# Kernel optimization log

Hardware: AMD Instinct MI355X
Metric: run time of the kernel (lower is better)

## Reference

```python
import jax, jax.numpy as jnp
import numpy as np

B, S, D, H, DH, SD = 4, 512, 768, 12, 64, 30
ALPHA, BETA = 1.0, 1.0


def setup_inputs() -> dict:
    root = jax.random.key(0)
    ks = jax.random.split(root, 16)
    n = lambda k, sh: jax.random.normal(k, sh, dtype=jnp.float32)
    w = lambda k, sh: 0.02 * jax.random.normal(k, sh, dtype=jnp.float32)
    return {
        "key": n(ks[0], (B, S, D)),
        "value": n(ks[1], (B, S, D)),
        "query": n(ks[2], (B, S, D)),
        "structure": n(ks[3], (B, S, S, SD)),
        "mask": jax.random.randint(ks[4], (B, S, S), 0, 2).astype(bool),
        "Wq": w(ks[5], (D, D)), "bq": jnp.zeros((D,), jnp.float32),
        "Wk": w(ks[6], (D, D)), "bk": jnp.zeros((D,), jnp.float32),
        "Wv": w(ks[7], (D, D)), "bv": jnp.zeros((D,), jnp.float32),
        "Wsk": w(ks[8], (SD, DH)), "bsk": jnp.zeros((DH,), jnp.float32),
        "Wsv": w(ks[9], (SD, DH)), "bsv": jnp.zeros((DH,), jnp.float32),
        "Wo": w(ks[10], (D, D)), "bo": jnp.zeros((D,), jnp.float32),
    }


def reference(key, value, query, structure, mask,
              Wq, bq, Wk, bk, Wv, bv, Wsk, bsk, Wsv, bsv, Wo, bo):
    # shape: [B,S,D] -> [B,H,S,DH]
    def proj(x, W, b):
        return (x @ W + b).reshape(B, -1, H, DH).transpose(0, 2, 1, 3)

    q = proj(query, Wq, bq) / np.float32(np.sqrt(DH))  # scale applied before both score terms
    k = proj(key, Wk, bk)
    v = proj(value, Wv, bv)

    sk = structure @ Wsk + bsk  # [B,Q,K,DH] relative-structure keys
    sv = structure @ Wsv + bsv  # [B,Q,K,DH] relative-structure values

    scores = jnp.einsum('bhqd,bhkd->bhqk', q, k)
    scores = scores + ALPHA * jnp.einsum('bhqd,bqkd->bhqk', q, sk)
    scores = jnp.where(mask[:, None, :, :], jnp.float32(-1e18), scores)

    attn = jax.nn.softmax(scores, axis=-1)  # dropout p=0 -> identity

    ctx = jnp.einsum('bhqk,bhkd->bhqd', attn, v)
    ctx = ctx + BETA * jnp.einsum('bhqk,bqkd->bhqd', attn, sv)
    ctx = ctx.transpose(0, 2, 1, 3).reshape(B, S, D)

    output = ctx @ Wo + bo
    top_attn = attn[:, 0]  # [B,Q,K]
    return output, top_attn
```

## Files before the change

### kernel.cpp

```cpp
#include <hip/hip_runtime.h>
#include <hip/hip_bf16.h>

typedef unsigned int uint32_ty;

typedef float  nfloat2 __attribute__((ext_vector_type(2)));
typedef float  nfloat4 __attribute__((ext_vector_type(4)));
typedef int    nint4   __attribute__((ext_vector_type(4)));
typedef short  bf16x8  __attribute__((ext_vector_type(8)));
typedef float  f32x4   __attribute__((ext_vector_type(4)));
typedef unsigned short ushort4n __attribute__((ext_vector_type(4)));

#define BB 4
#define SS 512
#define DD 768
#define HH 12
#define DHH 64
#define SDD 30

#define LP 520

__device__ __forceinline__ float bfu(unsigned short u) {
    return __uint_as_float(((uint32_ty)u) << 16);
}
__device__ __forceinline__ unsigned short tobf(float f) {
    return __bfloat16_as_ushort(__float2bfloat16(f));
}
__device__ __forceinline__ void unp8(uint4 u, float* t) {
    t[0] = __uint_as_float(u.x << 16);
    t[1] = __uint_as_float(u.x & 0xFFFF0000u);
    t[2] = __uint_as_float(u.y << 16);
    t[3] = __uint_as_float(u.y & 0xFFFF0000u);
    t[4] = __uint_as_float(u.z << 16);
    t[5] = __uint_as_float(u.z & 0xFFFF0000u);
    t[6] = __uint_as_float(u.w << 16);
    t[7] = __uint_as_float(u.w & 0xFFFF0000u);
}
__device__ __forceinline__ void unp4(uint2 u, float* t) {
    t[0] = __uint_as_float(u.x << 16);
    t[1] = __uint_as_float(u.x & 0xFFFF0000u);
    t[2] = __uint_as_float(u.y << 16);
    t[3] = __uint_as_float(u.y & 0xFFFF0000u);
}

#define MBM 64
#define MBN 64
#define MBK 64
#define LDK 72

__global__ __launch_bounds__(256) void gemm_proj3(
    const float* __restrict__ Xq, const float* __restrict__ Xk, const float* __restrict__ Xv,
    const float* __restrict__ Wq, const float* __restrict__ Wk, const float* __restrict__ Wv,
    const float* __restrict__ bq, const float* __restrict__ bk, const float* __restrict__ bv,
    float* __restrict__ oq, unsigned short* __restrict__ okT, unsigned short* __restrict__ ov)
{
    __shared__ unsigned short As[MBM][LDK];
    __shared__ unsigned short Bs[MBN][LDK];
    int z = blockIdx.z;
    const float* X = (z == 0) ? Xq : (z == 1) ? Xk : Xv;
    const float* W = (z == 0) ? Wq : (z == 1) ? Wk : Wv;
    const float* bias = (z == 0) ? bq : (z == 1) ? bk : bv;

    int tid = threadIdx.x;
    int lane = tid & 63, wave = tid >> 6;
    int m0 = blockIdx.y * MBM, n0 = blockIdx.x * MBN;
    int wm = (wave >> 1) * 32, wn = (wave & 1) * 32;
    int fr = lane & 15, fq = lane >> 4;

    f32x4 acc[2][2];
#pragma unroll
    for (int i = 0; i < 2; i++)
#pragma unroll
        for (int j = 0; j < 2; j++) acc[i][j] = (f32x4){0.f, 0.f, 0.f, 0.f};

    for (int k0 = 0; k0 < DD; k0 += MBK) {
#pragma unroll
        for (int rep = 0; rep < 4; rep++) {
            int i = tid + 256 * rep;
            int r = i >> 4, c4 = i & 15;
            float4 xv = *(const float4*)(X + (size_t)(m0 + r) * DD + k0 + 4 * c4);
            ushort4n pk = {tobf(xv.x), tobf(xv.y), tobf(xv.z), tobf(xv.w)};
            *(ushort4n*)&As[r][4 * c4] = pk;
        }
#pragma unroll
        for (int rep = 0; rep < 4; rep++) {
            int i = tid + 256 * rep;
            int r = i >> 4, c4 = i & 15;
            float4 wv = *(const float4*)(W + (size_t)(k0 + r) * DD + n0 + 4 * c4);
            Bs[4 * c4 + 0][r] = tobf(wv.x);
            Bs[4 * c4 + 1][r] = tobf(wv.y);
            Bs[4 * c4 + 2][r] = tobf(wv.z);
            Bs[4 * c4 + 3][r] = tobf(wv.w);
        }
        __syncthreads();
#pragma unroll
        for (int ks = 0; ks < 2; ks++) {
            bf16x8 a0 = *(bf16x8*)&As[wm + fr][ks * 32 + fq * 8];
            bf16x8 a1 = *(bf16x8*)&As[wm + 16 + fr][ks * 32 + fq * 8];
            bf16x8 b0 = *(bf16x8*)&Bs[wn + fr][ks * 32 + fq * 8];
            bf16x8 b1 = *(bf16x8*)&Bs[wn + 16 + fr][ks * 32 + fq * 8];
            acc[0][0] = __builtin_amdgcn_mfma_f32_16x16x32_bf16(a0, b0, acc[0][0], 0, 0, 0);
            acc[0][1] = __builtin_amdgcn_mfma_f32_16x16x32_bf16(a0, b1, acc[0][1], 0, 0, 0);
            acc[1][0] = __builtin_amdgcn_mfma_f32_16x16x32_bf16(a1, b0, acc[1][0], 0, 0, 0);
            acc[1][1] = __builtin_amdgcn_mfma_f32_16x16x32_bf16(a1, b1, acc[1][1], 0, 0, 0);
        }
        __syncthreads();
    }

#pragma unroll
    for (int i = 0; i < 2; i++) {
#pragma unroll
        for (int j = 0; j < 2; j++) {
            int n = n0 + wn + 16 * j + fr;
            int h = n >> 6, d = n & 63;
            float bn = bias[n];
            int mbase = m0 + wm + 16 * i + fq * 4;
            int b = mbase >> 9, sbase = mbase & 511;
            if (z == 1) {
                ushort4n pk;
#pragma unroll
                for (int r = 0; r < 4; r++) pk[r] = tobf(acc[i][j][r] + bn);
                *(ushort4n*)(okT + ((((size_t)b * HH + h) * DHH + d) * SS + sbase)) = pk;
            } else if (z == 0) {
#pragma unroll
                for (int r = 0; r < 4; r++)
                    oq[((((size_t)b * HH + h) * SS + sbase + r) * DHH + d)] =
                        (acc[i][j][r] + bn) * 0.125f;
            } else {
#pragma unroll
                for (int r = 0; r < 4; r++)
                    ov[((((size_t)b * HH + h) * SS + sbase + r) * DHH + d)] =
                        tobf(acc[i][j][r] + bn);
            }
        }
    }
}

__global__ __launch_bounds__(256) void gemm_out(
    const float* __restrict__ Xf, const float* __restrict__ W,
    const float* __restrict__ bias, float* __restrict__ out)
{
    __shared__ unsigned short As[MBM][LDK];
    __shared__ unsigned short Bs[MBN][LDK];
    int tid = threadIdx.x;
    int lane = tid & 63, wave = tid >> 6;
    int m0 = blockIdx.y * MBM, n0 = blockIdx.x * MBN;
    int wm = (wave >> 1) * 32, wn = (wave & 1) * 32;
    int fr = lane & 15, fq = lane >> 4;

    f32x4 acc[2][2];
#pragma unroll
    for (int i = 0; i < 2; i++)
#pragma unroll
        for (int j = 0; j < 2; j++) acc[i][j] = (f32x4){0.f, 0.f, 0.f, 0.f};

    for (int k0 = 0; k0 < DD; k0 += MBK) {
#pragma unroll
        for (int rep = 0; rep < 4; rep++) {
            int i = tid + 256 * rep;
            int r = i >> 4, c4 = i & 15;
            float4 xv = *(const float4*)(Xf + (size_t)(m0 + r) * DD + k0 + 4 * c4);
            ushort4n pk = {tobf(xv.x), tobf(xv.y), tobf(xv.z), tobf(xv.w)};
            *(ushort4n*)&As[r][4 * c4] = pk;
        }
#pragma unroll
        for (int rep = 0; rep < 4; rep++) {
            int i = tid + 256 * rep;
            int r = i >> 4, c4 = i & 15;
            float4 wv = *(const float4*)(W + (size_t)(k0 + r) * DD + n0 + 4 * c4);
            Bs[4 * c4 + 0][r] = tobf(wv.x);
            Bs[4 * c4 + 1][r] = tobf(wv.y);
            Bs[4 * c4 + 2][r] = tobf(wv.z);
            Bs[4 * c4 + 3][r] = tobf(wv.w);
        }
        __syncthreads();
#pragma unroll
        for (int ks = 0; ks < 2; ks++) {
            bf16x8 a0 = *(bf16x8*)&As[wm + fr][ks * 32 + fq * 8];
            bf16x8 a1 = *(bf16x8*)&As[wm + 16 + fr][ks * 32 + fq * 8];
            bf16x8 b0 = *(bf16x8*)&Bs[wn + fr][ks * 32 + fq * 8];
            bf16x8 b1 = *(bf16x8*)&Bs[wn + 16 + fr][ks * 32 + fq * 8];
            acc[0][0] = __builtin_amdgcn_mfma_f32_16x16x32_bf16(a0, b0, acc[0][0], 0, 0, 0);
            acc[0][1] = __builtin_amdgcn_mfma_f32_16x16x32_bf16(a0, b1, acc[0][1], 0, 0, 0);
            acc[1][0] = __builtin_amdgcn_mfma_f32_16x16x32_bf16(a1, b0, acc[1][0], 0, 0, 0);
            acc[1][1] = __builtin_amdgcn_mfma_f32_16x16x32_bf16(a1, b1, acc[1][1], 0, 0, 0);
        }
        __syncthreads();
    }

#pragma unroll
    for (int i = 0; i < 2; i++) {
#pragma unroll
        for (int j = 0; j < 2; j++) {
            int n = n0 + wn + 16 * j + fr;
            float bn = bias[n];
            int mbase = m0 + wm + 16 * i + fq * 4;
#pragma unroll
            for (int r = 0; r < 4; r++)
                out[(size_t)(mbase + r) * DD + n] = acc[i][j][r] + bn;
        }
    }
}

__global__ __launch_bounds__(256) void attn_fused(
    const float* __restrict__ q,
    const unsigned short* __restrict__ kT,
    const unsigned short* __restrict__ v,
    const float* __restrict__ structure,
    const int* __restrict__ mask,
    const float* __restrict__ Wsk,
    const float* __restrict__ bsk,
    const float* __restrict__ Wsv,
    const float* __restrict__ bsv,
    float* __restrict__ ctx,
    float* __restrict__ top_attn)
{
    __shared__ float qs[HH][DHH];
    __shared__ unsigned short stT[SDD][LP];
    __shared__ float qt_s[HH][SDD];
    __shared__ float qb_s[HH];
    __shared__ float astr_s[HH][SDD];
    __shared__ unsigned short at[HH][LP];

    int tid = threadIdx.x;
    int lane = tid & 63, wave = tid >> 6;

    int blk = blockIdx.x;
    int xcd = blk & 7;
    int b = xcd >> 1;
    int qp = ((xcd & 1) << 8) | (blk >> 3);

    for (int i = tid; i < HH * DHH; i += 256) {
        int h = i >> 6, d = i & 63;
        qs[h][d] = q[(((size_t)b * HH + h) * SS + qp) * DHH + d];
    }
    {
        const float* srow = structure + ((size_t)b * SS + qp) * (size_t)(SS * SDD);
        for (int k = tid; k < SS; k += 256) {
            const nfloat2* rp = (const nfloat2*)(srow + (size_t)k * SDD);
#pragma unroll
            for (int w = 0; w < 15; w++) {
                nfloat2 xv = __builtin_nontemporal_load(rp + w);
                stT[2 * w][k] = tobf(xv.x);
                stT[2 * w + 1][k] = tobf(xv.y);
            }
        }
    }
    __syncthreads();

    for (int i = tid; i < HH * SDD; i += 256) {
        int h = i / SDD, si = i % SDD;
        const float4* wp = (const float4*)(Wsk + si * DHH);
        const float4* qp4 = (const float4*)qs[h];
        float a = 0.f;
#pragma unroll
        for (int d4 = 0; d4 < 16; d4++) {
            float4 wv = wp[d4];
            float4 qv = qp4[d4];
            a += qv.x * wv.x + qv.y * wv.y + qv.z * wv.z + qv.w * wv.w;
        }
        qt_s[h][si] = a;
    }
    if (tid < HH) {
        const float4* bp = (const float4*)bsk;
        const float4* qp4 = (const float4*)qs[tid];
        float a = 0.f;
#pragma unroll
        for (int d4 = 0; d4 < 16; d4++) {
            float4 wv = bp[d4];
            float4 qv = qp4[d4];
            a += qv.x * wv.x + qv.y * wv.y + qv.z * wv.z + qv.w * wv.w;
        }
        qb_s[tid] = a;
    }
    __syncthreads();

    int h0 = wave * 3;
    float attnv[3][8];
#pragma unroll
    for (int h = 0; h < 3; h++)
#pragma unroll
        for (int j = 0; j < 8; j++) attnv[h][j] = 0.f;

#pragma unroll 2
    for (int si = 0; si < SDD; si++) {
        uint4 sv4 = *(const uint4*)&stT[si][8 * lane];
        float t[8];
        unp8(sv4, t);
#pragma unroll
        for (int h = 0; h < 3; h++) {
            float qt = qt_s[h0 + h][si];
#pragma unroll
            for (int j = 0; j < 8; j++) attnv[h][j] += qt * t[j];
        }
    }

    {
        const unsigned short* kbase = kT + (((size_t)b * HH + h0) * DHH) * SS + 8 * lane;
#pragma unroll
        for (int h = 0; h < 3; h++) {
            const unsigned short* kp = kbase + (size_t)h * (DHH * SS);
            float acc[8] = {0.f, 0.f, 0.f, 0.f, 0.f, 0.f, 0.f, 0.f};
#pragma unroll 8
            for (int d = 0; d < DHH; d++) {
                float qd = qs[h0 + h][d];
                uint4 kv = *(const uint4*)(kp + (size_t)d * SS);
                float t[8];
                unp8(kv, t);
#pragma unroll
                for (int j = 0; j < 8; j++) acc[j] += qd * t[j];
            }
            float qb = qb_s[h0 + h];
#pragma unroll
            for (int j = 0; j < 8; j++) attnv[h][j] += acc[j] + qb;
        }
    }

    {
        const int* mrow = mask + ((size_t)b * SS + qp) * SS + 8 * lane;
        nint4 m0v = __builtin_nontemporal_load((const nint4*)mrow);
        nint4 m1v = __builtin_nontemporal_load(((const nint4*)mrow) + 1);
        int mm[8] = {m0v.x, m0v.y, m0v.z, m0v.w, m1v.x, m1v.y, m1v.z, m1v.w};
#pragma unroll
        for (int h = 0; h < 3; h++)
#pragma unroll
            for (int j = 0; j < 8; j++)
                if (mm[j]) attnv[h][j] = -1e18f;
    }

#pragma unroll
    for (int h = 0; h < 3; h++) {
        float m = attnv[h][0];
#pragma unroll
        for (int j = 1; j < 8; j++) m = fmaxf(m, attnv[h][j]);
#pragma unroll
        for (int off = 32; off > 0; off >>= 1) m = fmaxf(m, __shfl_xor(m, off));
        float l = 0.f;
#pragma unroll
        for (int j = 0; j < 8; j++) { attnv[h][j] = __expf(attnv[h][j] - m); l += attnv[h][j]; }
#pragma unroll
        for (int off = 32; off > 0; off >>= 1) l += __shfl_xor(l, off);
        float inv = 1.f / l;
        float a[8];
#pragma unroll
        for (int j = 0; j < 8; j++) a[j] = attnv[h][j] * inv;
        uint4 pk;
        pk.x = (uint32_ty)tobf(a[0]) | ((uint32_ty)tobf(a[1]) << 16);
        pk.y = (uint32_ty)tobf(a[2]) | ((uint32_ty)tobf(a[3]) << 16);
        pk.z = (uint32_ty)tobf(a[4]) | ((uint32_ty)tobf(a[5]) << 16);
        pk.w = (uint32_ty)tobf(a[6]) | ((uint32_ty)tobf(a[7]) << 16);
        *(uint4*)&at[h0 + h][8 * lane] = pk;
        if (h0 + h == 0) {
            float* tp = top_attn + ((size_t)b * SS + qp) * SS + 8 * lane;
            nfloat4 w0 = {a[0], a[1], a[2], a[3]};
            nfloat4 w1 = {a[4], a[5], a[6], a[7]};
            __builtin_nontemporal_store(w0, (nfloat4*)tp);
            __builtin_nontemporal_store(w1, ((nfloat4*)tp) + 1);
        }
    }
    __syncthreads();

    if (tid < 180) {
        int h = tid / 15, sp = tid % 15;
        int si0 = 2 * sp, si1 = si0 + 1;
        float a0e = 0.f, a0o = 0.f, a1e = 0.f, a1o = 0.f;
#pragma unroll 2
        for (int j = 0; j < 64; j++) {
            uint4 av = *(const uint4*)&at[h][8 * j];
            uint4 s0 = *(const uint4*)&stT[si0][8 * j];
            uint4 s1 = *(const uint4*)&stT[si1][8 * j];
            float a[8], t0[8], t1[8];
            unp8(av, a); unp8(s0, t0); unp8(s1, t1);
#pragma unroll
            for (int t = 0; t < 8; t += 2) {
                a0e += a[t] * t0[t];     a0o += a[t + 1] * t0[t + 1];
                a1e += a[t] * t1[t];     a1o += a[t + 1] * t1[t + 1];
            }
        }
        astr_s[h][si0] = a0e + a0o;
        astr_s[h][si1] = a1e + a1o;
    }
    __syncthreads();

    if (tid < 192) {
        int h = tid >> 4, dq = tid & 15;
        const unsigned short* vp = v + ((size_t)b * HH + h) * (size_t)(SS * DHH) + 4 * dq;
        float4 ae; ae.x = ae.y = ae.z = ae.w = 0.f;
        float4 ao; ao.x = ao.y = ao.z = ao.w = 0.f;
#pragma unroll 2
        for (int j = 0; j < 64; j++) {
            uint4 av = *(const uint4*)&at[h][8 * j];
            float a[8];
            unp8(av, a);
            const unsigned short* vk = vp + (size_t)(8 * j) * DHH;
#pragma unroll
            for (int t = 0; t < 8; t += 2) {
                uint2 v0 = *(const uint2*)(vk + (size_t)t * DHH);
                uint2 v1 = *(const uint2*)(vk + (size_t)(t + 1) * DHH);
                float f0[4], f1[4];
                unp4(v0, f0); unp4(v1, f1);
                ae.x += a[t] * f0[0]; ae.y += a[t] * f0[1];
                ae.z += a[t] * f0[2]; ae.w += a[t] * f0[3];
                ao.x += a[t + 1] * f1[0]; ao.y += a[t + 1] * f1[1];
                ao.z += a[t + 1] * f1[2]; ao.w += a[t + 1] * f1[3];
            }
        }
        float4 sa = *(const float4*)(bsv + 4 * dq);
#pragma unroll
        for (int si = 0; si < SDD; si++) {
            float as = astr_s[h][si];
            float4 wv = *(const float4*)(Wsv + si * DHH + 4 * dq);
            sa.x += as * wv.x; sa.y += as * wv.y;
            sa.z += as * wv.z; sa.w += as * wv.w;
        }
        float4 outv;
        outv.x = ae.x + ao.x + sa.x;
        outv.y = ae.y + ao.y + sa.y;
        outv.z = ae.z + ao.z + sa.z;
        outv.w = ae.w + ao.w + sa.w;
        *(float4*)(ctx + ((size_t)b * SS + qp) * DD + h * DHH + 4 * dq) = outv;
    }
}

extern "C" void kernel_launch(void* const* d_in, const int* in_sizes, int n_in,
                              void* d_out, int out_size, void* d_ws, size_t ws_size,
                              hipStream_t stream)
{
    const float* key       = (const float*)d_in[0];
    const float* value     = (const float*)d_in[1];
    const float* query     = (const float*)d_in[2];
    const float* structure = (const float*)d_in[3];
    const int*   mask      = (const int*)d_in[4];
    const float* Wq  = (const float*)d_in[5];
    const float* bq  = (const float*)d_in[6];
    const float* Wk  = (const float*)d_in[7];
    const float* bk  = (const float*)d_in[8];
    const float* Wv  = (const float*)d_in[9];
    const float* bv  = (const float*)d_in[10];
    const float* Wsk = (const float*)d_in[11];
    const float* bsk = (const float*)d_in[12];
    const float* Wsv = (const float*)d_in[13];
    const float* bsv = (const float*)d_in[14];
    const float* Wo  = (const float*)d_in[15];
    const float* bo  = (const float*)d_in[16];

    float* out_main = (float*)d_out;
    float* out_attn = (float*)d_out + (size_t)BB * SS * DD;

    float* ws = (float*)d_ws;
    float*          q_buf   = ws;
    unsigned short* kT_buf  = (unsigned short*)(ws + 1572864);
    unsigned short* v_buf   = (unsigned short*)(ws + 2359296);
    float*          ctx_buf = ws + 3145728;

    dim3 ggrd3(DD / MBN, (BB * SS) / MBM, 3);
    gemm_proj3<<<ggrd3, dim3(256), 0, stream>>>(query, key, value, Wq, Wk, Wv,
                                                bq, bk, bv, q_buf, kT_buf, v_buf);

    attn_fused<<<BB * SS, 256, 0, stream>>>(q_buf, kT_buf, v_buf, structure, mask,
                                            Wsk, bsk, Wsv, bsv, ctx_buf, out_attn);

    dim3 ggrd(DD / MBN, (BB * SS) / MBM);
    gemm_out<<<ggrd, dim3(256), 0, stream>>>(ctx_buf, Wo, bo, out_main);
}
```

Before: 510.5 us.

## Pre-convert K/V inputs and weights to bf16 with transposed weights for GEMMs

Adds two pre-pass kernels. One converts the key and value activations to bf16. The other transposes and converts all four weight matrices to bf16 in an n-major layout. The projection and output GEMMs then load 16-byte bf16 vectors straight into shared memory instead of converting fp32 per element and doing scattered transposed shared-memory stores. The attention kernel now writes ctx as bf16, which halves its write and read traffic. The costs are two extra kernel launches and an extra full pass over K/V, plus reuse of the key buffer's workspace for ctx.

```diff
diff --git a/kernel.cpp b/kernel.cpp
--- a/kernel.cpp
+++ b/kernel.cpp
@@ -24,6 +24,9 @@
 }
 __device__ __forceinline__ unsigned short tobf(float f) {
     return __bfloat16_as_ushort(__float2bfloat16(f));
+}
+__device__ __forceinline__ uint32_ty pk2(float a, float b) {
+    return ((uint32_ty)tobf(a)) | ((uint32_ty)tobf(b) << 16);
 }
 __device__ __forceinline__ void unp8(uint4 u, float* t) {
     t[0] = __uint_as_float(u.x << 16);
@@ -42,22 +45,72 @@
     t[3] = __uint_as_float(u.y & 0xFFFF0000u);
 }
 
+__global__ __launch_bounds__(256) void cvt_x(
+    const float* __restrict__ k_in, const float* __restrict__ v_in,
+    unsigned short* __restrict__ kb, unsigned short* __restrict__ vb)
+{
+    const float* in = blockIdx.z ? v_in : k_in;
+    unsigned short* out = blockIdx.z ? vb : kb;
+    size_t i = (size_t)blockIdx.x * 256 + threadIdx.x;
+    const float4* p = (const float4*)in;
+    float4 a = p[2 * i], b = p[2 * i + 1];
+    uint4 pk;
+    pk.x = pk2(a.x, a.y); pk.y = pk2(a.z, a.w);
+    pk.z = pk2(b.x, b.y); pk.w = pk2(b.z, b.w);
+    ((uint4*)out)[i] = pk;
+}
+
+__global__ __launch_bounds__(256) void cvt_wT(
+    const float* __restrict__ W0, const float* __restrict__ W1,
+    const float* __restrict__ W2, const float* __restrict__ W3,
+    unsigned short* __restrict__ T0, unsigned short* __restrict__ T1,
+    unsigned short* __restrict__ T2, unsigned short* __restrict__ T3)
+{
+    __shared__ float tile[64][65];
+    int z = blockIdx.z;
+    const float* W = (z == 0) ? W0 : (z == 1) ? W1 : (z == 2) ? W2 : W3;
+    unsigned short* T = (z == 0) ? T0 : (z == 1) ? T1 : (z == 2) ? T2 : T3;
+    int k0 = blockIdx.y * 64, n0 = blockIdx.x * 64;
+    int tid = threadIdx.x;
+#pragma unroll
+    for (int rep = 0; rep < 4; rep++) {
+        int i = tid + 256 * rep;
+        int r = i >> 4, c4 = i & 15;
+        float4 wv = *(const float4*)(W + (size_t)(k0 + r) * DD + n0 + 4 * c4);
+        tile[r][4 * c4 + 0] = wv.x; tile[r][4 * c4 + 1] = wv.y;
+        tile[r][4 * c4 + 2] = wv.z; tile[r][4 * c4 + 3] = wv.w;
+    }
+    __syncthreads();
+#pragma unroll
+    for (int rep = 0; rep < 2; rep++) {
+        int i = tid + 256 * rep;
+        int n = i >> 3, kc = i & 7;
+        uint4 pk;
+        pk.x = pk2(tile[8 * kc + 0][n], tile[8 * kc + 1][n]);
+        pk.y = pk2(tile[8 * kc + 2][n], tile[8 * kc + 3][n]);
+        pk.z = pk2(tile[8 * kc + 4][n], tile[8 * kc + 5][n]);
+        pk.w = pk2(tile[8 * kc + 6][n], tile[8 * kc + 7][n]);
+        *(uint4*)(T + (size_t)(n0 + n) * DD + k0 + 8 * kc) = pk;
+    }
+}
+
 #define MBM 64
 #define MBN 64
 #define MBK 64
 #define LDK 72
 
 __global__ __launch_bounds__(256) void gemm_proj3(
-    const float* __restrict__ Xq, const float* __restrict__ Xk, const float* __restrict__ Xv,
-    const float* __restrict__ Wq, const float* __restrict__ Wk, const float* __restrict__ Wv,
+    const float* __restrict__ Xq,
+    const unsigned short* __restrict__ Xkb, const unsigned short* __restrict__ Xvb,
+    const unsigned short* __restrict__ WTq, const unsigned short* __restrict__ WTk,
+    const unsigned short* __restrict__ WTv,
     const float* __restrict__ bq, const float* __restrict__ bk, const float* __restrict__ bv,
     float* __restrict__ oq, unsigned short* __restrict__ okT, unsigned short* __restrict__ ov)
 {
     __shared__ unsigned short As[MBM][LDK];
     __shared__ unsigned short Bs[MBN][LDK];
     int z = blockIdx.z;
-    const float* X = (z == 0) ? Xq : (z == 1) ? Xk : Xv;
-    const float* W = (z == 0) ? Wq : (z == 1) ? Wk : Wv;
+    const unsigned short* WT = (z == 0) ? WTq : (z == 1) ? WTk : WTv;
     const float* bias = (z == 0) ? bq : (z == 1) ? bk : bv;
 
     int tid = threadIdx.x;
@@ -73,23 +126,31 @@
         for (int j = 0; j < 2; j++) acc[i][j] = (f32x4){0.f, 0.f, 0.f, 0.f};
 
     for (int k0 = 0; k0 < DD; k0 += MBK) {
-#pragma unroll
-        for (int rep = 0; rep < 4; rep++) {
+        if (z == 0) {
+#pragma unroll
+            for (int rep = 0; rep < 4; rep++) {
+                int i = tid + 256 * rep;
+                int r = i >> 4, c4 = i & 15;
+                float4 xv = *(const float4*)(Xq + (size_t)(m0 + r) * DD + k0 + 4 * c4);
+                ushort4n pk = {tobf(xv.x), tobf(xv.y), tobf(xv.z), tobf(xv.w)};
+                *(ushort4n*)&As[r][4 * c4] = pk;
+            }
+        } else {
+            const unsigned short* Xb = (z == 1) ? Xkb : Xvb;
+#pragma unroll
+            for (int rep = 0; rep < 2; rep++) {
+                int i = tid + 256 * rep;
+                int r = i >> 3, c = i & 7;
+                *(uint4*)&As[r][8 * c] =
+                    *(const uint4*)(Xb + (size_t)(m0 + r) * DD + k0 + 8 * c);
+            }
+        }
+#pragma unroll
+        for (int rep = 0; rep < 2; rep++) {
             int i = tid + 256 * rep;
-            int r = i >> 4, c4 = i & 15;
-            float4 xv = *(const float4*)(X + (size_t)(m0 + r) * DD + k0 + 4 * c4);
-            ushort4n pk = {tobf(xv.x), tobf(xv.y), tobf(xv.z), tobf(xv.w)};
-            *(ushort4n*)&As[r][4 * c4] = pk;
-        }
-#pragma unroll
-        for (int rep = 0; rep < 4; rep++) {
-            int i = tid + 256 * rep;
-            int r = i >> 4, c4 = i & 15;
-            float4 wv = *(const float4*)(W + (size_t)(k0 + r) * DD + n0 + 4 * c4);
-            Bs[4 * c4 + 0][r] = tobf(wv.x);
-            Bs[4 * c4 + 1][r] = tobf(wv.y);
-            Bs[4 * c4 + 2][r] = tobf(wv.z);
-            Bs[4 * c4 + 3][r] = tobf(wv.w);
+            int r = i >> 3, c = i & 7;
+            *(uint4*)&Bs[r][8 * c] =
+                *(const uint4*)(WT + (size_t)(n0 + r) * DD + k0 + 8 * c);
         }
         __syncthreads();
 #pragma unroll
@@ -136,7 +197,7 @@
 }
 
 __global__ __launch_bounds__(256) void gemm_out(
-    const float* __restrict__ Xf, const float* __restrict__ W,
+    const unsigned short* __restrict__ ctxb, const unsigned short* __restrict__ WoT,
     const float* __restrict__ bias, float* __restrict__ out)
 {
     __shared__ unsigned short As[MBM][LDK];
@@ -155,22 +216,18 @@
 
     for (int k0 = 0; k0 < DD; k0 += MBK) {
 #pragma unroll
-        for (int rep = 0; rep < 4; rep++) {
+        for (int rep = 0; rep < 2; rep++) {
             int i = tid + 256 * rep;
-            int r = i >> 4, c4 = i & 15;
-            float4 xv = *(const float4*)(Xf + (size_t)(m0 + r) * DD + k0 + 4 * c4);
-            ushort4n pk = {tobf(xv.x), tobf(xv.y), tobf(xv.z), tobf(xv.w)};
-            *(ushort4n*)&As[r][4 * c4] = pk;
-        }
-#pragma unroll
-        for (int rep = 0; rep < 4; rep++) {
+            int r = i >> 3, c = i & 7;
+            *(uint4*)&As[r][8 * c] =
+                *(const uint4*)(ctxb + (size_t)(m0 + r) * DD + k0 + 8 * c);
+        }
+#pragma unroll
+        for (int rep = 0; rep < 2; rep++) {
             int i = tid + 256 * rep;
-            int r = i >> 4, c4 = i & 15;
-            float4 wv = *(const float4*)(W + (size_t)(k0 + r) * DD + n0 + 4 * c4);
-            Bs[4 * c4 + 0][r] = tobf(wv.x);
-            Bs[4 * c4 + 1][r] = tobf(wv.y);
-            Bs[4 * c4 + 2][r] = tobf(wv.z);
-            Bs[4 * c4 + 3][r] = tobf(wv.w);
+            int r = i >> 3, c = i & 7;
+            *(uint4*)&Bs[r][8 * c] =
+                *(const uint4*)(WoT + (size_t)(n0 + r) * DD + k0 + 8 * c);
         }
         __syncthreads();
 #pragma unroll
@@ -211,7 +268,7 @@
     const float* __restrict__ bsk,
     const float* __restrict__ Wsv,
     const float* __restrict__ bsv,
-    float* __restrict__ ctx,
+    unsigned short* __restrict__ ctxb,
     float* __restrict__ top_attn)
 {
     __shared__ float qs[HH][DHH];
@@ -412,12 +469,12 @@
             sa.x += as * wv.x; sa.y += as * wv.y;
             sa.z += as * wv.z; sa.w += as * wv.w;
         }
-        float4 outv;
-        outv.x = ae.x + ao.x + sa.x;
-        outv.y = ae.y + ao.y + sa.y;
-        outv.z = ae.z + ao.z + sa.z;
-        outv.w = ae.w + ao.w + sa.w;
-        *(float4*)(ctx + ((size_t)b * SS + qp) * DD + h * DHH + 4 * dq) = outv;
+        ushort4n co;
+        co[0] = tobf(ae.x + ao.x + sa.x);
+        co[1] = tobf(ae.y + ao.y + sa.y);
+        co[2] = tobf(ae.z + ao.z + sa.z);
+        co[3] = tobf(ae.w + ao.w + sa.w);
+        *(ushort4n*)(ctxb + ((size_t)b * SS + qp) * DD + h * DHH + 4 * dq) = co;
     }
 }
 
@@ -446,19 +503,30 @@
     float* out_main = (float*)d_out;
     float* out_attn = (float*)d_out + (size_t)BB * SS * DD;
 
-    float* ws = (float*)d_ws;
-    float*          q_buf   = ws;
-    unsigned short* kT_buf  = (unsigned short*)(ws + 1572864);
-    unsigned short* v_buf   = (unsigned short*)(ws + 2359296);
-    float*          ctx_buf = ws + 3145728;
+    unsigned short* u = (unsigned short*)d_ws;
+    unsigned short* Xb_k  = u;
+    unsigned short* Xb_v  = u + 1572864;
+    unsigned short* WT_q  = u + 3145728;
+    unsigned short* WT_k  = u + 3735552;
+    unsigned short* WT_v  = u + 4325376;
+    unsigned short* WT_o  = u + 4915200;
+    unsigned short* kT_b  = u + 5505024;
+    unsigned short* v_b   = u + 7077888;
+    float*          q_buf = (float*)(u + 8650752);
+    unsigned short* ctx_b = Xb_k;
+
+    cvt_x<<<dim3(768, 1, 2), dim3(256), 0, stream>>>(key, value, Xb_k, Xb_v);
+    cvt_wT<<<dim3(12, 12, 4), dim3(256), 0, stream>>>(Wq, Wk, Wv, Wo,
+                                                      WT_q, WT_k, WT_v, WT_o);
 
     dim3 ggrd3(DD / MBN, (BB * SS) / MBM, 3);
-    gemm_proj3<<<ggrd3, dim3(256), 0, stream>>>(query, key, value, Wq, Wk, Wv,
-                                                bq, bk, bv, q_buf, kT_buf, v_buf);
-
-    attn_fused<<<BB * SS, 256, 0, stream>>>(q_buf, kT_buf, v_buf, structure, mask,
-                                            Wsk, bsk, Wsv, bsv, ctx_buf, out_attn);
+    gemm_proj3<<<ggrd3, dim3(256), 0, stream>>>(query, Xb_k, Xb_v,
+                                                WT_q, WT_k, WT_v,
+                                                bq, bk, bv, q_buf, kT_b, v_b);
+
+    attn_fused<<<BB * SS, 256, 0, stream>>>(q_buf, kT_b, v_b, structure, mask,
+                                            Wsk, bsk, Wsv, bsv, ctx_b, out_attn);
 
     dim3 ggrd(DD / MBN, (BB * SS) / MBM);
-    gemm_out<<<ggrd, dim3(256), 0, stream>>>(ctx_buf, Wo, bo, out_main);
-}
+    gemm_out<<<ggrd, dim3(256), 0, stream>>>(ctx_b, WT_o, bo, out_main);
+}
```

New measurement: 476.5 us. 6.7% less time.
